# Optimization experiments

Measured on AMD Instinct MI355X. Metric: run time of the kernel, lower is better.

The kernel has to match this reference:

```python
import jax, jax.numpy as jnp
import numpy as np

WSCALE = 0.05  # keep qk logits in a stable range for softmax

def setup_inputs() -> dict:
    key = jax.random.key(0)
    ks = jax.random.split(key, 7)
    B, C, H, W = 8, 256, 64, 64
    d = C // 8
    x = jax.random.normal(ks[0], (B, C, H, W), dtype=jnp.float32)
    Wq = jax.random.normal(ks[1], (d, C), dtype=jnp.float32) * WSCALE
    Wk = jax.random.normal(ks[2], (d, C), dtype=jnp.float32) * WSCALE
    Wv = jax.random.normal(ks[3], (C, C), dtype=jnp.float32) * WSCALE
    bq = jnp.zeros((d,), jnp.float32)
    bk = jnp.zeros((d,), jnp.float32)
    bv = jnp.zeros((C,), jnp.float32)
    return {"x": x, "Wq": Wq, "bq": bq, "Wk": Wk, "bk": bk, "Wv": Wv, "bv": bv}

def reference(x, Wq, bq, Wk, bk, Wv, bv):
    B, C, H, W = x.shape
    N = H * W
    xf = x.reshape(B, C, N)                                  # [B,C,N]
    # 1x1 convs == per-pixel linear projections
    q = jnp.einsum('dc,bcn->bdn', Wq, xf) + bq[None, :, None]  # [B,d,N]
    k = jnp.einsum('dc,bcn->bdn', Wk, xf) + bk[None, :, None]  # [B,d,N]
    v = jnp.einsum('ec,bcn->ben', Wv, xf) + bv[None, :, None]  # [B,C,N]
    # attn[b,i,j] = q_i . k_j ; softmax over j (keys)
    attn = jax.nn.softmax(jnp.einsum('bdi,bdj->bij', q, k), axis=-1)  # [B,N,N]
    # out[b,c,i] = sum_j v[b,c,j] * attn[b,i,j]
    out = jnp.einsum('bcj,bij->bci', v, attn)                # [B,C,N]
    return out.reshape(B, C, H, W)
```

## Files before the change

### kernel.cpp

```cpp
#include <hip/hip_runtime.h>
#include <math.h>

#define NB 8
#define NC 256
#define ND 32
#define NN 4096
#define NM 320
#define LOG2E 1.44269504088896f
#define XSTR 264

typedef short short8 __attribute__((ext_vector_type(8)));
typedef float f32x4 __attribute__((ext_vector_type(4)));

__device__ __forceinline__ unsigned int f2bf_u(float f) {
    return (__float_as_uint(f) + 0x8000u) >> 16;
}
__device__ __forceinline__ unsigned short f2bf(float f) {
    return (unsigned short)f2bf_u(f);
}

__global__ __launch_bounds__(256) void repack_kernel(
    const float* __restrict__ Wq, const float* __restrict__ bq,
    const float* __restrict__ Wk, const float* __restrict__ bk,
    const float* __restrict__ Wv, const float* __restrict__ bv,
    unsigned short* __restrict__ wp, float* __restrict__ bias)
{
    const int T    = blockIdx.x * 256 + threadIdx.x;
    const int j    = T & 7;
    const int lane = (T >> 3) & 63;
    const int ks   = (T >> 9) & 7;
    const int mt   = T >> 12;
    const int m = mt * 16 + (lane & 15);
    const int k = ks * 32 + ((lane >> 4) << 3) + j;
    float wv;
    if (m < 32)       wv = Wq[m * NC + k] * LOG2E;
    else if (m < 64)  wv = Wk[(m - 32) * NC + k];
    else              wv = Wv[(m - 64) * NC + k];
    wp[T] = f2bf(wv);
    if (T < NM) {
        float bb;
        if (T < 32)      bb = bq[T] * LOG2E;
        else if (T < 64) bb = bk[T - 32];
        else             bb = bv[T - 64];
        bias[T] = bb;
    }
}

__global__ __launch_bounds__(256, 4) void proj_kernel(
    const float* __restrict__ x,
    const unsigned short* __restrict__ wp,
    const float* __restrict__ bias,
    unsigned short* __restrict__ q_ws,
    unsigned short* __restrict__ k_ws,
    unsigned short* __restrict__ v_ws)
{
    __shared__ __align__(16) unsigned short xs[32 * XSTR];

    const int b  = blockIdx.x >> 7;
    const int n0 = (blockIdx.x & 127) << 5;
    const int t  = threadIdx.x;

    {
        const int n  = t & 31;
        const int cg = t >> 5;
        const float* xb = x + (size_t)b * NC * NN + n0 + n;
        #pragma unroll
        for (int it = 0; it < 8; ++it) {
            const int c = 32 * it + 4 * cg;
            const float x0 = xb[(size_t)(c + 0) * NN];
            const float x1 = xb[(size_t)(c + 1) * NN];
            const float x2 = xb[(size_t)(c + 2) * NN];
            const float x3 = xb[(size_t)(c + 3) * NN];
            uint2 pk;
            pk.x = (f2bf_u(x1) << 16) | f2bf_u(x0);
            pk.y = (f2bf_u(x3) << 16) | f2bf_u(x2);
            *(uint2*)(xs + n * XSTR + c) = pk;
        }
    }
    __syncthreads();

    const int w    = t >> 6;
    const int lane = t & 63;
    const int li = lane & 15;
    const int qd = lane >> 4;

    f32x4 acc[5][2];
    #pragma unroll
    for (int u = 0; u < 5; ++u) {
        const int mt = w + 4 * u;
        const f32x4 b4 = *(const f32x4*)(bias + mt * 16 + qd * 4);
        acc[u][0] = b4; acc[u][1] = b4;
    }

    #pragma unroll
    for (int ks = 0; ks < 8; ++ks) {
        short8 bf[2];
        #pragma unroll
        for (int nf = 0; nf < 2; ++nf)
            bf[nf] = *(const short8*)(xs + (nf * 16 + li) * XSTR + ks * 32 + qd * 8);
        #pragma unroll
        for (int u = 0; u < 5; ++u) {
            const int mt = w + 4 * u;
            const short8 af = *(const short8*)(wp + (size_t)((mt * 8 + ks) * 64 + lane) * 8);
            acc[u][0] = __builtin_amdgcn_mfma_f32_16x16x32_bf16(af, bf[0], acc[u][0], 0, 0, 0);
            acc[u][1] = __builtin_amdgcn_mfma_f32_16x16x32_bf16(af, bf[1], acc[u][1], 0, 0, 0);
        }
    }

    #pragma unroll
    for (int u = 0; u < 5; ++u) {
        const int mt = w + 4 * u;
        if (mt < 4) {
            unsigned short* dst = (mt < 2) ? q_ws : k_ws;
            const int d0 = (mt & 1) * 16 + qd * 4;
            #pragma unroll
            for (int nf = 0; nf < 2; ++nf) {
                const int n = n0 + nf * 16 + li;
                uint2 pk;
                pk.x = (f2bf_u(acc[u][nf][1]) << 16) | f2bf_u(acc[u][nf][0]);
                pk.y = (f2bf_u(acc[u][nf][3]) << 16) | f2bf_u(acc[u][nf][2]);
                *(uint2*)(dst + ((size_t)b * NN + n) * ND + d0) = pk;
            }
        } else {
            const int c0 = (mt - 4) * 16 + qd * 4;
            #pragma unroll
            for (int nf = 0; nf < 2; ++nf) {
                const int n = n0 + nf * 16 + li;
                #pragma unroll
                for (int r = 0; r < 4; ++r)
                    v_ws[((size_t)b * NC + c0 + r) * NN + n] = f2bf(acc[u][nf][r]);
            }
        }
    }
}

__global__ __launch_bounds__(512, 4) void attn_kernel(
    const unsigned short* __restrict__ q_ws,
    const unsigned short* __restrict__ k_ws,
    const unsigned short* __restrict__ v_ws,
    float* __restrict__ out)
{
    __shared__ __align__(16) unsigned short Pb[2][4][16 * 64];
    __shared__ float lred[8][16];

    const int b  = blockIdx.x & 7;
    const int i0 = (blockIdx.x >> 3) * 64;
    const int t  = threadIdx.x;
    const int w    = t >> 6;
    const int lane = t & 63;
    const int li = lane & 15;
    const int qd = lane >> 4;
    const int sw = w & 3;
    const int th = w >> 2;
    const int c0 = w * 32;
    const int rot = (li & 3) << 2;

    const int wblk0 = ((8 * th + 0 + qd) + rot) & 15;
    const int wblk1 = ((8 * th + 4 + qd) + rot) & 15;
    const int rblk0 = ((2 * qd) + rot) & 15;
    const int rblk1 = ((8 + 2 * qd) + rot) & 15;

    const short8 qf = *(const short8*)(q_ws + ((size_t)b * NN + i0 + 16 * sw + li) * ND + qd * 8);
    const unsigned short* kb = k_ws + (size_t)b * NN * ND + (size_t)li * ND + qd * 8
                             + (size_t)(16 * 2 * th) * ND;
    const unsigned short* vb0 = v_ws + ((size_t)b * NC + c0 + li) * NN + qd * 8;
    const unsigned short* vb1 = vb0 + (size_t)16 * NN;

    f32x4 o[4][2];
    #pragma unroll
    for (int sb = 0; sb < 4; ++sb) { o[sb][0] = (f32x4){0,0,0,0}; o[sb][1] = (f32x4){0,0,0,0}; }
    float l_loc = 0.f;
    const f32x4 z4 = {0.f, 0.f, 0.f, 0.f};

    int buf = 0;
    for (int j0 = 0; j0 < NN; j0 += 64) {
        const short8 kf0 = *(const short8*)(kb + (size_t)j0 * ND);
        const short8 kf1 = *(const short8*)(kb + (size_t)(j0 + 16) * ND);
        short8 vf[2][2];
        #pragma unroll
        for (int ks = 0; ks < 2; ++ks) {
            vf[0][ks] = *(const short8*)(vb0 + j0 + 32 * ks);
            vf[1][ks] = *(const short8*)(vb1 + j0 + 32 * ks);
        }

        unsigned short* Pw = &Pb[buf][sw][li * 64];
        #pragma unroll
        for (int tt = 0; tt < 2; ++tt) {
            const f32x4 s = __builtin_amdgcn_mfma_f32_16x16x32_bf16(tt ? kf1 : kf0, qf, z4, 0, 0, 0);
            const float p0 = __builtin_amdgcn_exp2f(s[0]);
            const float p1 = __builtin_amdgcn_exp2f(s[1]);
            const float p2 = __builtin_amdgcn_exp2f(s[2]);
            const float p3 = __builtin_amdgcn_exp2f(s[3]);
            l_loc += (p0 + p1) + (p2 + p3);
            const unsigned u0 = __float_as_uint(p0) + 0x8000u;
            const unsigned u1 = __float_as_uint(p1) + 0x8000u;
            const unsigned u2 = __float_as_uint(p2) + 0x8000u;
            const unsigned u3 = __float_as_uint(p3) + 0x8000u;
            uint2 pk;
            pk.x = __builtin_amdgcn_perm(u1, u0, 0x07060302u);
            pk.y = __builtin_amdgcn_perm(u3, u2, 0x07060302u);
            *(uint2*)(Pw + (tt ? wblk1 : wblk0) * 4) = pk;
        }

        __syncthreads();

        #pragma unroll
        for (int sb = 0; sb < 4; ++sb) {
            const unsigned short* Pr = &Pb[buf][sb][li * 64];
            const short8 pf0 = *(const short8*)(Pr + rblk0 * 4);
            const short8 pf1 = *(const short8*)(Pr + rblk1 * 4);
            o[sb][0] = __builtin_amdgcn_mfma_f32_16x16x32_bf16(vf[0][0], pf0, o[sb][0], 0, 0, 0);
            o[sb][0] = __builtin_amdgcn_mfma_f32_16x16x32_bf16(vf[0][1], pf1, o[sb][0], 0, 0, 0);
            o[sb][1] = __builtin_amdgcn_mfma_f32_16x16x32_bf16(vf[1][0], pf0, o[sb][1], 0, 0, 0);
            o[sb][1] = __builtin_amdgcn_mfma_f32_16x16x32_bf16(vf[1][1], pf1, o[sb][1], 0, 0, 0);
        }
        buf ^= 1;
    }

    l_loc += __shfl_xor(l_loc, 16, 64);
    l_loc += __shfl_xor(l_loc, 32, 64);
    if (lane < 16) lred[w][lane] = l_loc;
    __syncthreads();
    float linv[4];
    #pragma unroll
    for (int sb = 0; sb < 4; ++sb)
        linv[sb] = 1.0f / (lred[sb][li] + lred[sb + 4][li]);

    #pragma unroll
    for (int sb = 0; sb < 4; ++sb)
        #pragma unroll
        for (int nt = 0; nt < 2; ++nt) {
            const int c = c0 + nt * 16 + qd * 4;
            float* op = out + ((size_t)b * NC + c) * NN + i0 + 16 * sb + li;
            #pragma unroll
            for (int r = 0; r < 4; ++r)
                op[(size_t)r * NN] = o[sb][nt][r] * linv[sb];
        }
}

extern "C" void kernel_launch(void* const* d_in, const int* in_sizes, int n_in,
                              void* d_out, int out_size, void* d_ws, size_t ws_size,
                              hipStream_t stream) {
    const float* x  = (const float*)d_in[0];
    const float* Wq = (const float*)d_in[1];
    const float* bq = (const float*)d_in[2];
    const float* Wk = (const float*)d_in[3];
    const float* bk = (const float*)d_in[4];
    const float* Wv = (const float*)d_in[5];
    const float* bv = (const float*)d_in[6];
    float* out = (float*)d_out;

    unsigned short* q_ws = (unsigned short*)d_ws;
    unsigned short* k_ws = q_ws + (size_t)NB * NN * ND;
    unsigned short* v_ws = k_ws + (size_t)NB * NN * ND;
    unsigned short* wp   = v_ws + (size_t)NB * NC * NN;
    float*          bias = (float*)(wp + (size_t)NM * NC);

    repack_kernel<<<NM * NC / 256, 256, 0, stream>>>(Wq, bq, Wk, bk, Wv, bv, wp, bias);
    proj_kernel<<<NB * (NN / 32), 256, 0, stream>>>(x, wp, bias, q_ws, k_ws, v_ws);
    attn_kernel<<<NB * (NN / 64), 512, 0, stream>>>(q_ws, k_ws, v_ws, out);
}
```

Before: 248.8 us.

## Split attention blocks by channel half and software-pipeline S and PV stages

Result: slower. 277.1 us (+11.4%).

```diff
diff --git a/kernel.cpp b/kernel.cpp
--- a/kernel.cpp
+++ b/kernel.cpp
@@ -134,37 +134,36 @@
     }
 }
 
-__global__ __launch_bounds__(512, 4) void attn_kernel(
+__global__ __launch_bounds__(256, 4) void attn_kernel(
     const unsigned short* __restrict__ q_ws,
     const unsigned short* __restrict__ k_ws,
     const unsigned short* __restrict__ v_ws,
     float* __restrict__ out)
 {
-    __shared__ __align__(16) unsigned short Pb[2][4][16 * 64];
-    __shared__ float lred[8][16];
-
-    const int b  = blockIdx.x & 7;
-    const int i0 = (blockIdx.x >> 3) * 64;
-    const int t  = threadIdx.x;
-    const int w    = t >> 6;
-    const int lane = t & 63;
+    __shared__ __align__(16) unsigned short Pb[2][4 * 16 * 64];
+    __shared__ float lred[4][16];
+
+    const int b   = blockIdx.x & 7;
+    const int idx = blockIdx.x >> 3;
+    const int i0  = (idx >> 1) * 64;
+    const int ch  = (idx & 1) * 128;
+    const int w    = threadIdx.x >> 6;
+    const int lane = threadIdx.x & 63;
     const int li = lane & 15;
     const int qd = lane >> 4;
-    const int sw = w & 3;
-    const int th = w >> 2;
-    const int c0 = w * 32;
     const int rot = (li & 3) << 2;
-
-    const int wblk0 = ((8 * th + 0 + qd) + rot) & 15;
-    const int wblk1 = ((8 * th + 4 + qd) + rot) & 15;
-    const int rblk0 = ((2 * qd) + rot) & 15;
-    const int rblk1 = ((8 + 2 * qd) + rot) & 15;
-
-    const short8 qf = *(const short8*)(q_ws + ((size_t)b * NN + i0 + 16 * sw + li) * ND + qd * 8);
-    const unsigned short* kb = k_ws + (size_t)b * NN * ND + (size_t)li * ND + qd * 8
-                             + (size_t)(16 * 2 * th) * ND;
+    const int c0 = ch + w * 32;
+
+    const int rpos0 = (2 * qd + rot) & 15;
+    const int rpos1 = (8 + 2 * qd + rot) & 15;
+
+    const short8 qf = *(const short8*)(q_ws + ((size_t)b * NN + i0 + 16 * w + li) * ND + qd * 8);
+    const unsigned short* kb  = k_ws + ((size_t)b * NN + li) * ND + qd * 8;
     const unsigned short* vb0 = v_ws + ((size_t)b * NC + c0 + li) * NN + qd * 8;
     const unsigned short* vb1 = vb0 + (size_t)16 * NN;
+
+    unsigned short* PA = &Pb[0][0];
+    unsigned short* PB = &Pb[1][0];
 
     f32x4 o[4][2];
     #pragma unroll
@@ -172,21 +171,24 @@
     float l_loc = 0.f;
     const f32x4 z4 = {0.f, 0.f, 0.f, 0.f};
 
-    int buf = 0;
-    for (int j0 = 0; j0 < NN; j0 += 64) {
-        const short8 kf0 = *(const short8*)(kb + (size_t)j0 * ND);
-        const short8 kf1 = *(const short8*)(kb + (size_t)(j0 + 16) * ND);
-        short8 vf[2][2];
-        #pragma unroll
-        for (int ks = 0; ks < 2; ++ks) {
-            vf[0][ks] = *(const short8*)(vb0 + j0 + 32 * ks);
-            vf[1][ks] = *(const short8*)(vb1 + j0 + 32 * ks);
-        }
-
-        unsigned short* Pw = &Pb[buf][sw][li * 64];
-        #pragma unroll
-        for (int tt = 0; tt < 2; ++tt) {
-            const f32x4 s = __builtin_amdgcn_mfma_f32_16x16x32_bf16(tt ? kf1 : kf0, qf, z4, 0, 0, 0);
+    short8 kf[4], vfA[2][2], vfB[2][2];
+
+    auto LKF = [&](int j0) {
+        #pragma unroll
+        for (int tt = 0; tt < 4; ++tt)
+            kf[tt] = *(const short8*)(kb + (size_t)(j0 + 16 * tt) * ND);
+    };
+    auto LVF = [&](int j0, short8 (&vf)[2][2]) {
+        vf[0][0] = *(const short8*)(vb0 + j0);
+        vf[0][1] = *(const short8*)(vb0 + j0 + 32);
+        vf[1][0] = *(const short8*)(vb1 + j0);
+        vf[1][1] = *(const short8*)(vb1 + j0 + 32);
+    };
+    auto DOS = [&](unsigned short* P) {
+        unsigned short* Pw = P + (w * 16 + li) * 64;
+        #pragma unroll
+        for (int tt = 0; tt < 4; ++tt) {
+            const f32x4 s = __builtin_amdgcn_mfma_f32_16x16x32_bf16(kf[tt], qf, z4, 0, 0, 0);
             const float p0 = __builtin_amdgcn_exp2f(s[0]);
             const float p1 = __builtin_amdgcn_exp2f(s[1]);
             const float p2 = __builtin_amdgcn_exp2f(s[2]);
@@ -199,42 +201,63 @@
             uint2 pk;
             pk.x = __builtin_amdgcn_perm(u1, u0, 0x07060302u);
             pk.y = __builtin_amdgcn_perm(u3, u2, 0x07060302u);
-            *(uint2*)(Pw + (tt ? wblk1 : wblk0) * 4) = pk;
-        }
-
-        __syncthreads();
-
+            const int wp = (4 * tt + qd + rot) & 15;
+            *(uint2*)(Pw + wp * 4) = pk;
+        }
+    };
+    auto DOPV = [&](const unsigned short* P, const short8 (&vf)[2][2]) {
         #pragma unroll
         for (int sb = 0; sb < 4; ++sb) {
-            const unsigned short* Pr = &Pb[buf][sb][li * 64];
-            const short8 pf0 = *(const short8*)(Pr + rblk0 * 4);
-            const short8 pf1 = *(const short8*)(Pr + rblk1 * 4);
+            const unsigned short* Pr = P + (sb * 16 + li) * 64;
+            const short8 pf0 = *(const short8*)(Pr + rpos0 * 4);
+            const short8 pf1 = *(const short8*)(Pr + rpos1 * 4);
             o[sb][0] = __builtin_amdgcn_mfma_f32_16x16x32_bf16(vf[0][0], pf0, o[sb][0], 0, 0, 0);
             o[sb][0] = __builtin_amdgcn_mfma_f32_16x16x32_bf16(vf[0][1], pf1, o[sb][0], 0, 0, 0);
             o[sb][1] = __builtin_amdgcn_mfma_f32_16x16x32_bf16(vf[1][0], pf0, o[sb][1], 0, 0, 0);
             o[sb][1] = __builtin_amdgcn_mfma_f32_16x16x32_bf16(vf[1][1], pf1, o[sb][1], 0, 0, 0);
         }
-        buf ^= 1;
-    }
+    };
+
+    LKF(0); LVF(0, vfA);
+    DOS(PA);
+    __syncthreads();
+    int j0 = 64;
+    for (int it = 0; it < 31; ++it) {
+        LKF(j0); LVF(j0, vfB);
+        DOPV(PA, vfA);
+        DOS(PB);
+        __syncthreads();
+        j0 += 64;
+        LKF(j0); LVF(j0, vfA);
+        DOPV(PB, vfB);
+        DOS(PA);
+        __syncthreads();
+        j0 += 64;
+    }
+    LKF(j0); LVF(j0, vfB);
+    DOPV(PA, vfA);
+    DOS(PB);
+    __syncthreads();
+    DOPV(PB, vfB);
 
     l_loc += __shfl_xor(l_loc, 16, 64);
     l_loc += __shfl_xor(l_loc, 32, 64);
-    if (lane < 16) lred[w][lane] = l_loc;
+    if (lane < 16) lred[w][li] = l_loc;
     __syncthreads();
     float linv[4];
     #pragma unroll
     for (int sb = 0; sb < 4; ++sb)
-        linv[sb] = 1.0f / (lred[sb][li] + lred[sb + 4][li]);
+        linv[sb] = 1.0f / lred[sb][li];
 
     #pragma unroll
     for (int sb = 0; sb < 4; ++sb)
         #pragma unroll
-        for (int nt = 0; nt < 2; ++nt) {
-            const int c = c0 + nt * 16 + qd * 4;
+        for (int ct = 0; ct < 2; ++ct) {
+            const int c = c0 + ct * 16 + qd * 4;
             float* op = out + ((size_t)b * NC + c) * NN + i0 + 16 * sb + li;
             #pragma unroll
             for (int r = 0; r < 4; ++r)
-                op[(size_t)r * NN] = o[sb][nt][r] * linv[sb];
+                op[(size_t)r * NN] = o[sb][ct][r] * linv[sb];
         }
 }
 
@@ -258,5 +281,5 @@
 
     repack_kernel<<<NM * NC / 256, 256, 0, stream>>>(Wq, bq, Wk, bk, Wv, bv, wp, bias);
     proj_kernel<<<NB * (NN / 32), 256, 0, stream>>>(x, wp, bias, q_ws, k_ws, v_ws);
-    attn_kernel<<<NB * (NN / 64), 512, 0, stream>>>(q_ws, k_ws, v_ws, out);
-}
+    attn_kernel<<<NB * (NN / 64) * 2, 256, 0, stream>>>(q_ws, k_ws, v_ws, out);
+}
```
